# Performance work log

Measured on AMD Instinct MI355X. Metric: run time of the kernel, lower is better.

## Reference

```python
import jax, jax.numpy as jnp
import numpy as np

N = 96                       # max_num_nodes
T = N * (N + 1) // 2         # upper-triangular vector length
E = 256                      # embedding_dim
MAX_ITERS = 50


def setup_inputs() -> dict:
    key = jax.random.key(0)
    ks = jax.random.split(key, 8)
    graph_embedding = jax.random.normal(ks[0], (1, E), jnp.float32)
    a = (jax.random.uniform(ks[1], (1, N, N)) < 0.1).astype(jnp.float32)
    adj = jnp.maximum(a, jnp.swapaxes(a, 1, 2))  # symmetric 0/1 adjacency
    mask = jnp.ones((1, N), bool)
    W1 = jax.random.normal(ks[2], (E, 250), jnp.float32) * 0.08
    b1 = jnp.zeros((250,), jnp.float32)
    W2 = jax.random.normal(ks[3], (250, 100), jnp.float32) * 0.10
    b2 = jnp.zeros((100,), jnp.float32)
    W3 = jax.random.normal(ks[4], (100, T), jnp.float32) * 0.15
    b3 = jnp.zeros((T,), jnp.float32)
    return dict(graph_embedding=graph_embedding, adj=adj, mask=mask,
                W1=W1, b1=b1, W2=W2, b2=b2, W3=W3, b3=b3)


def _forward(graph_embedding, adj, mask, W1, b1, W2, b2, W3, b3):
    idx = jnp.arange(N)
    eye = jnp.eye(N, dtype=adj.dtype)

    # decoder: Linear -> Linear -> ReLU -> Linear -> sigmoid
    h = graph_embedding @ W1 + b1
    h = jax.nn.relu(h @ W2 + b2)
    l = jax.nn.sigmoid(h @ W3 + b3)[0]              # [T]

    # recover_adj_lower + recover_full_adj_from_lower
    iu = jnp.triu_indices(N)
    up = jnp.zeros((N, N), l.dtype).at[iu].set(l)    # row-major triu fill, as torch bool-mask assign
    recon = up + up.T - jnp.diag(jnp.diag(up))       # [N, N]
    fr = recon.sum(axis=1)                           # recon degree features

    # ori_adj with diagonal forced to 1 where mask
    a0 = adj[0]
    m = mask[0]
    ori = a0.at[idx, idx].set(jnp.where(m, jnp.asarray(1.0, a0.dtype), jnp.diag(a0)))
    f = ori.sum(axis=1)                              # ori degree features

    # edge_similarity_matrix, vectorized
    # off-diagonal block: S[i,j,a,b] = A[i,j]A[i,i]A[j,j] * R[a,b]R[a,a]R[b,b]  (i!=j, a!=b)
    dA = jnp.diag(ori)
    dR = jnp.diag(recon)
    t1 = (1.0 - eye) * ori * dA[:, None] * dA[None, :]      # [N, N], zero on diag
    t2 = (1.0 - eye) * recon * dR[:, None] * dR[None, :]    # [N, N], zero on diag
    S = t1[:, :, None, None] * t2[None, None, :, :]          # [N, N, N, N]
    # diagonal block: S[i,i,a,a] = A[i,i]R[a,a] / (|f_i - fr_a| + 1)
    sim = 1.0 / (jnp.abs(f[:, None] - fr[None, :]) + 1.0)    # [N, N]
    D = dA[:, None] * dR[None, :] * sim                      # [N, N]
    S = S.at[idx[:, None], idx[:, None], idx[None, :], idx[None, :]].set(D)

    # mpm: iterative max-pooling matching
    x0 = jnp.full((N, N), 1.0 / N, dtype=S.dtype)
    off_mask = (1.0 - eye)[:, :, None]                       # exclude j == i

    def step(x, _):
        pooled = jnp.max(x[None, :, None, :] * S, axis=3)    # [i, j, a] = max_b x[j,b]*S[i,j,a,b]
        neigh = (off_mask * pooled).sum(axis=1)              # [i, a]
        x_new = x * D + neigh                                # D[i,a] == S[i,i,a,a]
        x_new = x_new / jnp.linalg.norm(x_new)
        return x_new, None

    x, _ = jax.lax.scan(step, x0, None, length=MAX_ITERS)
    return x  # soft assignment matrix [N, N]


def reference(graph_embedding, adj, mask, W1, b1, W2, b2, W3, b3):
    return _forward(graph_embedding, adj, mask, W1, b1, W2, b2, W3, b3)
```

## Files before the change

### kernel.cpp

```cpp
#include <hip/hip_runtime.h>
#include <hip/hip_bf16.h>

#define NN 96
#define NB 16
#define NTH 512
#define RPB 6
#define OP2 288
#define NITER 50
#define SMASK 0x8000000080000000ULL
#define SPIN_MAX 32768

typedef unsigned long long ull;
typedef float v2f __attribute__((ext_vector_type(2)));

__device__ __forceinline__ float bf2f(__hip_bfloat16 v){ return __bfloat162float(v); }
__device__ __forceinline__ float LD(const void* p, int i, bool f32){
  return f32 ? ((const float*)p)[i]
             : __bfloat162float(((const __hip_bfloat16*)p)[i]);
}
__device__ __forceinline__ float ldA(const float* p){
  return __hip_atomic_load(p, __ATOMIC_RELAXED, __HIP_MEMORY_SCOPE_AGENT);
}
__device__ __forceinline__ void stA(float* p, float v){
  __hip_atomic_store(p, v, __ATOMIC_RELAXED, __HIP_MEMORY_SCOPE_AGENT);
}
__device__ __forceinline__ ull ldA64(const ull* p){
  return __hip_atomic_load(p, __ATOMIC_RELAXED, __HIP_MEMORY_SCOPE_AGENT);
}
__device__ __forceinline__ void stA64(ull* p, ull v){
  __hip_atomic_store(p, v, __ATOMIC_RELAXED, __HIP_MEMORY_SCOPE_AGENT);
}

__global__ __launch_bounds__(NTH, 1) void gvae(
    const void* __restrict__ ge,  const void* __restrict__ adj,
    const void* __restrict__ W1,  const void* __restrict__ b1,
    const void* __restrict__ W2,  const void* __restrict__ b2,
    const void* __restrict__ W3,  const void* __restrict__ b3,
    void* __restrict__ out, float* __restrict__ ws)
{
  __shared__ __align__(16) float t2s[NN * NN];
  __shared__ __align__(16) float Ms[NN * NN];
  __shared__ __align__(16) float xs[RPB * NN];
  __shared__ __align__(16) float Ds[RPB * NN];
  __shared__ float ges[256], h1s[250], h2s[100];
  __shared__ unsigned char nbl[RPB * 96];
  __shared__ int   ncnt[RPB];
  __shared__ float fdeg[RPB];
  __shared__ float frs[NN], dRs[NN];
  __shared__ float wred[8];
  __shared__ float s_sh;
  __shared__ int   bdone;

  const int tid = threadIdx.x, blk = blockIdx.x;

  if (blk >= NB){
    if (tid == 0) bdone = 0;
    __syncthreads();
    const float* dn = ws + 960;
    const int wv = tid >> 6;
    float a0 = 1.1f + blk, a1 = 2.2f, a2 = 3.3f, a3 = 4.4f;
    float a4 = 5.5f, a5 = 6.6f, a6 = 7.7f, a7 = 8.8f;
    const float m = 1.0000001f;
    for (int outer = 0; outer < 8192; ++outer){
#pragma unroll
      for (int u = 0; u < 64; ++u){
        a0 = fmaf(a0, m, 1e-6f); a1 = fmaf(a1, m, 2e-6f);
        a2 = fmaf(a2, m, 3e-6f); a3 = fmaf(a3, m, 4e-6f);
        a4 = fmaf(a4, m, 5e-6f); a5 = fmaf(a5, m, 6e-6f);
        a6 = fmaf(a6, m, 7e-6f); a7 = fmaf(a7, m, 8e-6f);
      }
      int stop;
      if (wv == 0){
        float v = (tid == 0) ? ldA(dn) : 0.f;
        stop = __any(v > 0.5f) ? 1 : 0;
        if (stop && tid == 0)
          __hip_atomic_store(&bdone, 1, __ATOMIC_RELAXED, __HIP_MEMORY_SCOPE_WORKGROUP);
      } else {
        stop = __hip_atomic_load(&bdone, __ATOMIC_RELAXED, __HIP_MEMORY_SCOPE_WORKGROUP);
      }
      if (stop) break;
    }
    float sum = a0 + a1 + a2 + a3 + a4 + a5 + a6 + a7;
    if (sum == 0.12345678f) stA(ws + 1016, sum);
    return;
  }

  float sv = (tid < 128) ? bf2f(((const __hip_bfloat16*)W1)[tid])
                         : bf2f(((const __hip_bfloat16*)W3)[tid - 128]);
  const bool isf32 = __syncthreads_or(!(fabsf(sv) < 1e4f)) != 0;

  float* pn  = ws;
  float* lg  = ws + 1024;
  ull*   Mb0 = (ull*)(ws + 8192);
  ull*   Mb1 = Mb0 + 4608;

  if (tid < 256) ges[tid] = LD(ge, tid, isf32);
  __syncthreads();
  if (tid < 250){
    float a0 = LD(b1, tid, isf32), a1 = 0.f, a2 = 0.f, a3 = 0.f;
    for (int e = 0; e < 256; e += 4){
      a0 += ges[e]     * LD(W1, (e    ) * 250 + tid, isf32);
      a1 += ges[e + 1] * LD(W1, (e + 1) * 250 + tid, isf32);
      a2 += ges[e + 2] * LD(W1, (e + 2) * 250 + tid, isf32);
      a3 += ges[e + 3] * LD(W1, (e + 3) * 250 + tid, isf32);
    }
    h1s[tid] = (a0 + a1) + (a2 + a3);
  }
  __syncthreads();
  if (tid < 100){
    float a0 = LD(b2, tid, isf32), a1 = 0.f;
    for (int k = 0; k < 250; k += 2){
      a0 += h1s[k]     * LD(W2, (k    ) * 100 + tid, isf32);
      a1 += h1s[k + 1] * LD(W2, (k + 1) * 100 + tid, isf32);
    }
    h2s[tid] = fmaxf(a0 + a1, 0.f);
  }
  __syncthreads();

  if (tid < 291){
    int o = blk * 291 + tid;
    float a = LD(b3, o, isf32);
    for (int k = 0; k < 100; ++k) a += h2s[k] * LD(W3, k * 4656 + o, isf32);
    stA(&lg[o], 1.f / (1.f + expf(-a)));
  }
  if (tid >= 448 && tid < 448 + RPB){
    int r = tid - 448, ig = blk * RPB + r;
    float fs = 1.f; int c = 0;
    for (int j = 0; j < NN; ++j){
      if (j == ig) continue;
      float v = LD(adj, ig * NN + j, isf32);
      fs += v;
      if (v > 0.5f) nbl[r * 96 + (c++)] = (unsigned char)j;
    }
    ncnt[r] = c; fdeg[r] = fs;
  }
  {
    float vv[10];
    unsigned pend = 0;
#pragma unroll
    for (int c = 0; c < 10; ++c) if (tid + NTH * c < 4656) pend |= 1u << c;
    int spin = 0;
    while (pend && spin++ < SPIN_MAX){
      unsigned p2 = pend;
#pragma unroll
      for (int c = 0; c < 10; ++c)
        if ((p2 >> c) & 1) vv[c] = ldA(&lg[tid + NTH * c]);
#pragma unroll
      for (int c = 0; c < 10; ++c)
        if (((p2 >> c) & 1) && vv[c] > 0.f){
          Ms[tid + NTH * c] = vv[c];
          pend &= ~(1u << c);
        }
    }
  }
  __syncthreads();

  for (int e = tid; e < NN * NN; e += NTH){
    int a = e / NN, b = e % NN, i = min(a, b), j = max(a, b);
    int k = i * NN - (i * (i - 1)) / 2 + (j - i);
    t2s[e] = Ms[k];
  }
  __syncthreads();
  if (tid < NN){
    float srow = 0.f;
    for (int b = 0; b < NN; ++b) srow += t2s[b * NN + tid];
    frs[tid] = srow; dRs[tid] = t2s[tid * NN + tid];
  }
  __syncthreads();
  for (int e = tid; e < NN * NN; e += NTH){
    int a = e / NN, b = e % NN;
    t2s[e] = (a == b) ? 0.f : t2s[e] * dRs[a] * dRs[b];
  }
  for (int o = tid; o < RPB * NN; o += NTH){
    int r = o / NN, a = o % NN;
    Ds[o] = dRs[a] / (fabsf(fdeg[r] - frs[a]) + 1.f);
    xs[o] = 1.f / 96.f;
  }
  __syncthreads();

  unsigned pend0 = 0;
  if (tid >= 256){
    int t2i = tid - 256;
#pragma unroll
    for (int e = 0; e < 18; ++e){
      int row = (t2i + 256 * e) / 48;
      if (row < blk * RPB || row >= blk * RPB + RPB) pend0 |= 1u << e;
    }
  }

  for (int it = 0; it < NITER; ++it){
    ull* Mw = (it & 1) ? Mb1 : Mb0;
    const ull sg = ((it >> 1) & 1) ? SMASK : 0ULL;

    if (tid < 256){
      for (int o = tid; o < OP2; o += 256){
        int r = o / 48, p = o % 48;
        const float* xr = &xs[r * NN];
        v2f m0 = {0.f, 0.f}, m1 = {0.f, 0.f};
        for (int b = 0; b < NN; b += 2){
          v2f t0 = *(const v2f*)&t2s[(b    ) * NN + 2 * p];
          v2f t1 = *(const v2f*)&t2s[(b + 1) * NN + 2 * p];
          float x0 = xr[b], x1 = xr[b + 1];
          m0.x = fmaxf(m0.x, x0 * t0.x); m0.y = fmaxf(m0.y, x0 * t0.y);
          m1.x = fmaxf(m1.x, x1 * t1.x); m1.y = fmaxf(m1.y, x1 * t1.y);
        }
        float mx = fmaxf(m0.x, m1.x), my = fmaxf(m0.y, m1.y);
        *(v2f*)&Ms[(blk * RPB + r) * NN + 2 * p] = (v2f){mx, my};
        ull enc = (((ull)__float_as_uint(my + 1.f)) << 32) | __float_as_uint(mx + 1.f);
        stA64(&Mw[(blk * RPB + r) * 48 + p], enc ^ sg);
      }
    } else {
      int t2i = tid - 256;
      if (it >= 2 && t2i < 64){
        float v = 0.f;
        if (t2i < 16){
          int sp = 0;
          do { v = ldA(&pn[(it - 1) * 16 + t2i]); }
          while (!(v > 0.f) && ++sp < SPIN_MAX);
        }
        for (int off = 8; off; off >>= 1) v += __shfl_down(v, off, 64);
        if (t2i == 0) s_sh = rsqrtf(v);
      }
      ull v[18];
      unsigned pend = pend0;
      int spin = 0;
      while (pend && spin++ < SPIN_MAX){
        unsigned p2 = pend;
#pragma unroll
        for (int e = 0; e < 18; ++e)
          if ((p2 >> e) & 1) v[e] = ldA64(&Mw[t2i + 256 * e]);
#pragma unroll
        for (int e = 0; e < 18; ++e)
          if (((p2 >> e) & 1) && !((v[e] ^ sg) & SMASK)){
            int c = t2i + 256 * e;
            Ms[2 * c]     = fabsf(__uint_as_float((unsigned)v[e])) - 1.f;
            Ms[2 * c + 1] = fabsf(__uint_as_float((unsigned)(v[e] >> 32))) - 1.f;
            pend &= ~(1u << e);
          }
      }
    }
    __syncthreads();

    float s = (it < 2) ? 1.f : s_sh;
    float nsq = 0.f;
    if (tid < OP2){
      int r = tid / 48, p = tid % 48;
      v2f acc = {0.f, 0.f};
      int cnt = ncnt[r];
      const unsigned char* nb = &nbl[r * 96];
      for (int c = 0; c < cnt; ++c){
        v2f mv = *(const v2f*)&Ms[nb[c] * NN + 2 * p];
        acc.x += mv.x; acc.y += mv.y;
      }
      v2f w2 = *(const v2f*)&xs[r * NN + 2 * p];
      v2f d2 = *(const v2f*)&Ds[r * NN + 2 * p];
      v2f u; u.x = s * (w2.x * d2.x + acc.x); u.y = s * (w2.y * d2.y + acc.y);
      *(v2f*)&xs[r * NN + 2 * p] = u;
      nsq = u.x * u.x + u.y * u.y;
    }
    for (int off = 32; off; off >>= 1) nsq += __shfl_down(nsq, off, 64);
    if ((tid & 63) == 0) wred[tid >> 6] = nsq;
    __syncthreads();
    if (tid == 0){
      float t = 0.f;
#pragma unroll
      for (int w = 0; w < 8; ++w) t += wred[w];
      stA(&pn[(it + 1) * 16 + blk], t);
    }
    __syncthreads();
  }

  if (tid < 16){
    float v; int sp = 0;
    do { v = ldA(&pn[NITER * 16 + tid]); } while (!(v > 0.f) && ++sp < SPIN_MAX);
    for (int off = 8; off; off >>= 1) v += __shfl_down(v, off, 64);
    if (tid == 0) s_sh = rsqrtf(v);
  }
  __syncthreads();
  float sf = s_sh;
  for (int o = tid; o < RPB * NN; o += NTH){
    int og = blk * RPB * NN + o;
    float v = sf * xs[o];
    if (isf32) ((float*)out)[og] = v;
    else       ((__hip_bfloat16*)out)[og] = __float2bfloat16(v);
  }
  if (blk == 0 && tid == 0) stA(ws + 960, 1.f);
}

extern "C" void kernel_launch(void* const* d_in, const int* in_sizes, int n_in,
                              void* d_out, int out_size, void* d_ws, size_t ws_size,
                              hipStream_t stream) {
  (void)in_sizes; (void)n_in; (void)out_size; (void)ws_size;
  hipLaunchKernelGGL(gvae, dim3(256), dim3(NTH), 0, stream,
                     d_in[0], d_in[1], d_in[3], d_in[4], d_in[5], d_in[6],
                     d_in[7], d_in[8], d_out, (float*)d_ws);
}
```

Before: 471.6 us.

## Poll only needed neighbor rows, drop per-iteration barrier, add sleep backoff

The polling warps now fetch only the remote rows of the pooled matrix that this block's rows actually neighbor, using a bitmask of needed rows built while reading the adjacency. Polling threads shrink to 192 and producer threads to 320, and the producers run at raised wave priority. The per-block norm publish moves to the start of the next iteration, which removes one block-wide barrier per iteration. Spin loops gain s_sleep backoff to cut memory-polling contention, at the risk of adding latency when data arrives just after a sleep starts.

New measurement: 441.3 us. 6.4% less time.

```diff
diff --git a/kernel.cpp b/kernel.cpp
--- a/kernel.cpp
+++ b/kernel.cpp
@@ -9,6 +9,8 @@
 #define NITER 50
 #define SMASK 0x8000000080000000ULL
 #define SPIN_MAX 32768
+#define PTH 192
+#define NCHK 24
 
 typedef unsigned long long ull;
 typedef float v2f __attribute__((ext_vector_type(2)));
@@ -47,6 +49,7 @@
   __shared__ int   ncnt[RPB];
   __shared__ float fdeg[RPB];
   __shared__ float frs[NN], dRs[NN];
+  __shared__ unsigned int nbits[3];
   __shared__ float wred[8];
   __shared__ float s_sh;
   __shared__ int   bdone;
@@ -85,6 +88,7 @@
     return;
   }
 
+  if (tid < 3) nbits[tid] = 0u;
   float sv = (tid < 128) ? bf2f(((const __hip_bfloat16*)W1)[tid])
                          : bf2f(((const __hip_bfloat16*)W3)[tid - 128]);
   const bool isf32 = __syncthreads_or(!(fabsf(sv) < 1e4f)) != 0;
@@ -130,7 +134,10 @@
       if (j == ig) continue;
       float v = LD(adj, ig * NN + j, isf32);
       fs += v;
-      if (v > 0.5f) nbl[r * 96 + (c++)] = (unsigned char)j;
+      if (v > 0.5f){
+        nbl[r * 96 + (c++)] = (unsigned char)j;
+        atomicOr(&nbits[j >> 5], 1u << (j & 31));
+      }
     }
     ncnt[r] = c; fdeg[r] = fs;
   }
@@ -151,6 +158,7 @@
           Ms[tid + NTH * c] = vv[c];
           pend &= ~(1u << c);
         }
+      if (pend == p2) __builtin_amdgcn_s_sleep(2);
     }
   }
   __syncthreads();
@@ -179,12 +187,14 @@
   __syncthreads();
 
   unsigned pend0 = 0;
-  if (tid >= 256){
-    int t2i = tid - 256;
-#pragma unroll
-    for (int e = 0; e < 18; ++e){
-      int row = (t2i + 256 * e) / 48;
-      if (row < blk * RPB || row >= blk * RPB + RPB) pend0 |= 1u << e;
+  if (tid >= NTH - PTH){
+    int pt = tid - (NTH - PTH);
+#pragma unroll
+    for (int e = 0; e < NCHK; ++e){
+      int row = (pt + PTH * e) / 48;
+      bool own  = (row >= blk * RPB) && (row < blk * RPB + RPB);
+      bool need = (nbits[row >> 5] >> (row & 31)) & 1u;
+      if (!own && need) pend0 |= 1u << e;
     }
   }
 
@@ -192,9 +202,17 @@
     ull* Mw = (it & 1) ? Mb1 : Mb0;
     const ull sg = ((it >> 1) & 1) ? SMASK : 0ULL;
 
-    if (tid < 256){
-      for (int o = tid; o < OP2; o += 256){
-        int r = o / 48, p = o % 48;
+    if (tid == 0 && it > 0){
+      float t = 0.f;
+#pragma unroll
+      for (int w = 0; w < 8; ++w) t += wred[w];
+      stA(&pn[it * 16 + blk], t);
+    }
+
+    if (tid < NTH - PTH){
+      __builtin_amdgcn_s_setprio(1);
+      if (tid < OP2){
+        int r = tid / 48, p = tid - r * 48;
         const float* xr = &xs[r * NN];
         v2f m0 = {0.f, 0.f}, m1 = {0.f, 0.f};
         for (int b = 0; b < NN; b += 2){
@@ -209,34 +227,40 @@
         ull enc = (((ull)__float_as_uint(my + 1.f)) << 32) | __float_as_uint(mx + 1.f);
         stA64(&Mw[(blk * RPB + r) * 48 + p], enc ^ sg);
       }
+      __builtin_amdgcn_s_setprio(0);
     } else {
-      int t2i = tid - 256;
-      if (it >= 2 && t2i < 64){
+      int pt = tid - (NTH - PTH);
+      if (it >= 2 && pt < 64){
         float v = 0.f;
-        if (t2i < 16){
+        if (pt < 16){
           int sp = 0;
-          do { v = ldA(&pn[(it - 1) * 16 + t2i]); }
-          while (!(v > 0.f) && ++sp < SPIN_MAX);
+          for (;;){
+            v = ldA(&pn[(it - 1) * 16 + pt]);
+            if (v > 0.f || ++sp >= SPIN_MAX) break;
+            __builtin_amdgcn_s_sleep(1);
+          }
         }
         for (int off = 8; off; off >>= 1) v += __shfl_down(v, off, 64);
-        if (t2i == 0) s_sh = rsqrtf(v);
-      }
-      ull v[18];
+        if (pt == 0) s_sh = rsqrtf(v);
+      }
+      ull v[NCHK];
       unsigned pend = pend0;
       int spin = 0;
       while (pend && spin++ < SPIN_MAX){
         unsigned p2 = pend;
 #pragma unroll
-        for (int e = 0; e < 18; ++e)
-          if ((p2 >> e) & 1) v[e] = ldA64(&Mw[t2i + 256 * e]);
-#pragma unroll
-        for (int e = 0; e < 18; ++e)
+        for (int e = 0; e < NCHK; ++e)
+          if ((p2 >> e) & 1) v[e] = ldA64(&Mw[pt + PTH * e]);
+#pragma unroll
+        for (int e = 0; e < NCHK; ++e)
           if (((p2 >> e) & 1) && !((v[e] ^ sg) & SMASK)){
-            int c = t2i + 256 * e;
-            Ms[2 * c]     = fabsf(__uint_as_float((unsigned)v[e])) - 1.f;
-            Ms[2 * c + 1] = fabsf(__uint_as_float((unsigned)(v[e] >> 32))) - 1.f;
+            int c = pt + PTH * e;
+            *(v2f*)&Ms[2 * c] =
+              (v2f){ fabsf(__uint_as_float((unsigned)v[e])) - 1.f,
+                     fabsf(__uint_as_float((unsigned)(v[e] >> 32))) - 1.f };
             pend &= ~(1u << e);
           }
+        if (pend == p2) __builtin_amdgcn_s_sleep(2);
       }
     }
     __syncthreads();
@@ -244,7 +268,7 @@
     float s = (it < 2) ? 1.f : s_sh;
     float nsq = 0.f;
     if (tid < OP2){
-      int r = tid / 48, p = tid % 48;
+      int r = tid / 48, p = tid - r * 48;
       v2f acc = {0.f, 0.f};
       int cnt = ncnt[r];
       const unsigned char* nb = &nbl[r * 96];
@@ -261,18 +285,21 @@
     for (int off = 32; off; off >>= 1) nsq += __shfl_down(nsq, off, 64);
     if ((tid & 63) == 0) wred[tid >> 6] = nsq;
     __syncthreads();
-    if (tid == 0){
-      float t = 0.f;
-#pragma unroll
-      for (int w = 0; w < 8; ++w) t += wred[w];
-      stA(&pn[(it + 1) * 16 + blk], t);
-    }
-    __syncthreads();
-  }
-
+  }
+
+  if (tid == 0){
+    float t = 0.f;
+#pragma unroll
+    for (int w = 0; w < 8; ++w) t += wred[w];
+    stA(&pn[NITER * 16 + blk], t);
+  }
   if (tid < 16){
     float v; int sp = 0;
-    do { v = ldA(&pn[NITER * 16 + tid]); } while (!(v > 0.f) && ++sp < SPIN_MAX);
+    for (;;){
+      v = ldA(&pn[NITER * 16 + tid]);
+      if (v > 0.f || ++sp >= SPIN_MAX) break;
+      __builtin_amdgcn_s_sleep(1);
+    }
     for (int off = 8; off; off >>= 1) v += __shfl_down(v, off, 64);
     if (tid == 0) s_sh = rsqrtf(v);
   }
```
